# Performance work log

Hardware: AMD Instinct MI355X
Metric: run time of the kernel (lower is better)

## Reference

```python
import jax, jax.numpy as jnp
import numpy as np

N, F_IN, H = 8192, 128, 256
AVG_DEG_P = 16.0 / N  # ~16 neighbors per node, BA-graph-like sparsity


def setup_inputs() -> dict:
    key = jax.random.key(0)
    ks = jax.random.split(key, 16)
    # symmetric 0/1 adjacency, no self-loops
    B = jax.random.bernoulli(ks[0], AVG_DEG_P, (N, N)).astype(jnp.float32)
    A = jnp.maximum(B, B.T)
    A = A * (1.0 - jnp.eye(N, dtype=jnp.float32))
    features = jax.random.normal(ks[1], (N, F_IN), dtype=jnp.float32)
    treatments = jax.random.bernoulli(ks[2], 0.1, (N, 1)).astype(jnp.float32)
    def glorot(k, shape):
        lim = float(np.sqrt(6.0 / (shape[0] + shape[1])))
        return jax.random.uniform(k, shape, jnp.float32, -lim, lim)
    return {
        "A": A,
        "features": features,
        "treatments": treatments,
        "W1": glorot(ks[3], (F_IN, H)),   # GCNConv layer 1 weight
        "b1": jnp.zeros((H,), jnp.float32),
        "W2": glorot(ks[4], (H, H)),      # GCNConv layer 2 weight
        "b2": jnp.zeros((H,), jnp.float32),
        "W_emb": glorot(ks[5], (H + 1, H)),
        "b_emb": jnp.zeros((H,), jnp.float32),
        "W_t0": glorot(ks[6], (H, 1)),
        "b_t0": jnp.zeros((1,), jnp.float32),
        "W_t1": glorot(ks[7], (H, 1)),
        "b_t1": jnp.zeros((1,), jnp.float32),
    }


def _gcn_norm(A):
    # PyG GCNConv default: D^-1/2 (A + I) D^-1/2
    A_hat = A + jnp.eye(A.shape[0], dtype=A.dtype)
    d = jnp.sum(A_hat, axis=1)
    dinv = jnp.where(d > 0, 1.0 / jnp.sqrt(d), 0.0)
    return A_hat * dinv[:, None] * dinv[None, :]


def reference(A, features, treatments, W1, b1, W2, b2, W_emb, b_emb, W_t0, b_t0, W_t1, b_t1):
    nA = _gcn_norm(A)                                  # [N, N]
    h = jax.nn.relu(nA @ (features @ W1) + b1)         # GCNConv 1, [N, H]
    h = jax.nn.relu(nA @ (h @ W2) + b2)                # GCNConv 2, [N, H]
    deg = jnp.sum(A, axis=1) + 1e-8                    # [N]
    # faithful to torch: (A * treatments).sum(dim=1) broadcasts treatments[N,1] over columns
    exposure = (jnp.sum(A * treatments, axis=1) / deg)[:, None]  # [N, 1]
    rep = jnp.concatenate([h, exposure], axis=1)       # [N, H+1]
    emb = jax.nn.relu(rep @ W_emb + b_emb)             # [N, H]
    y0_pred = (emb @ W_t0 + b_t0).reshape(-1)          # [N]
    y1_pred = (emb @ W_t1 + b_t1).reshape(-1)          # [N]
    return (y0_pred, y1_pred, emb)
```

## Files before the change

### kernel.cpp

```cpp
#include <hip/hip_runtime.h>

#define NN   8192
#define FIN  128
#define HH   256
#define CAP  128

__global__ __launch_bounds__(256) void k_build(
    const float* __restrict__ A, const float* __restrict__ treat,
    int* __restrict__ cols, int* __restrict__ cnt,
    float* __restrict__ dinv, float* __restrict__ expo)
{
  const int row = blockIdx.x;
  const float4* Ar = reinterpret_cast<const float4*>(A + (size_t)row * NN);
  __shared__ int s_cnt;
  __shared__ float s_rs[4];
  if (threadIdx.x == 0) s_cnt = 0;
  __syncthreads();

  float rs = 0.f;
  int* myCols = cols + (size_t)row * CAP;
  #pragma unroll
  for (int it = 0; it < NN / 4 / 256; ++it) {
    const int idx = it * 256 + threadIdx.x;
    const float4 a = Ar[idx];
    const int base = idx * 4;
    const float av[4] = {a.x, a.y, a.z, a.w};
    #pragma unroll
    for (int u = 0; u < 4; ++u) {
      if (av[u] != 0.0f) {
        rs += av[u];
        int p = atomicAdd(&s_cnt, 1);
        if (p < CAP) myCols[p] = base + u;
      }
    }
  }
  #pragma unroll
  for (int off = 32; off > 0; off >>= 1) rs += __shfl_down(rs, off);
  const int wid = threadIdx.x >> 6;
  if ((threadIdx.x & 63) == 0) s_rs[wid] = rs;
  __syncthreads();
  if (threadIdx.x == 0) {
    const float R = s_rs[0] + s_rs[1] + s_rs[2] + s_rs[3];
    int n = s_cnt; if (n > CAP) n = CAP;
    cnt[row]  = n;
    dinv[row] = rsqrtf(R + 1.0f);
    expo[row] = treat[row] * R / (R + 1e-8f);
  }
}

template<int K, bool EXPO>
__global__ __launch_bounds__(256) void k_gemm(
    const float* __restrict__ M, const float* __restrict__ W,
    const float* __restrict__ bias, const float* __restrict__ expo,
    float* __restrict__ out)
{
  constexpr int BM = 128, BN = 64, KT = 16;
  __shared__ float As[KT][BM];
  __shared__ float Bs[KT][BN];
  const int tid = threadIdx.x;
  const int tx = tid & 15;
  const int ty = tid >> 4;
  const int r0 = blockIdx.x * BM;
  const int c0 = blockIdx.y * BN;

  float acc[8][4];
  #pragma unroll
  for (int i = 0; i < 8; ++i)
    #pragma unroll
    for (int j = 0; j < 4; ++j) acc[i][j] = 0.f;

  const int lr = tid >> 1;
  const int lk = (tid & 1) * 8;
  const int bk = tid >> 4;
  const int bc = (tid & 15) * 4;

  for (int k0 = 0; k0 < K; k0 += KT) {
    const float4 a0 = *reinterpret_cast<const float4*>(&M[(size_t)(r0 + lr) * K + k0 + lk]);
    const float4 a1 = *reinterpret_cast<const float4*>(&M[(size_t)(r0 + lr) * K + k0 + lk + 4]);
    const float4 b0 = *reinterpret_cast<const float4*>(&W[(size_t)(k0 + bk) * HH + c0 + bc]);
    __syncthreads();
    As[lk + 0][lr] = a0.x; As[lk + 1][lr] = a0.y; As[lk + 2][lr] = a0.z; As[lk + 3][lr] = a0.w;
    As[lk + 4][lr] = a1.x; As[lk + 5][lr] = a1.y; As[lk + 6][lr] = a1.z; As[lk + 7][lr] = a1.w;
    *reinterpret_cast<float4*>(&Bs[bk][bc]) = b0;
    __syncthreads();
    #pragma unroll
    for (int kk = 0; kk < KT; ++kk) {
      const float4 av0 = *reinterpret_cast<const float4*>(&As[kk][ty * 8]);
      const float4 av1 = *reinterpret_cast<const float4*>(&As[kk][ty * 8 + 4]);
      const float4 bv  = *reinterpret_cast<const float4*>(&Bs[kk][tx * 4]);
      const float ar[8] = {av0.x, av0.y, av0.z, av0.w, av1.x, av1.y, av1.z, av1.w};
      const float br[4] = {bv.x, bv.y, bv.z, bv.w};
      #pragma unroll
      for (int i = 0; i < 8; ++i)
        #pragma unroll
        for (int j = 0; j < 4; ++j)
          acc[i][j] += ar[i] * br[j];
    }
  }

  float eb[4] = {0, 0, 0, 0}, bs[4] = {0, 0, 0, 0};
  if constexpr (EXPO) {
    const float4 we = *reinterpret_cast<const float4*>(&W[(size_t)K * HH + c0 + tx * 4]);
    eb[0] = we.x; eb[1] = we.y; eb[2] = we.z; eb[3] = we.w;
    const float4 bv = *reinterpret_cast<const float4*>(&bias[c0 + tx * 4]);
    bs[0] = bv.x; bs[1] = bv.y; bs[2] = bv.z; bs[3] = bv.w;
  }
  #pragma unroll
  for (int i = 0; i < 8; ++i) {
    const int r = r0 + ty * 8 + i;
    float4 o;
    float ov[4];
    if constexpr (EXPO) {
      const float e = expo[r];
      #pragma unroll
      for (int j = 0; j < 4; ++j) ov[j] = fmaxf(acc[i][j] + e * eb[j] + bs[j], 0.f);
    } else {
      #pragma unroll
      for (int j = 0; j < 4; ++j) ov[j] = acc[i][j];
    }
    o.x = ov[0]; o.y = ov[1]; o.z = ov[2]; o.w = ov[3];
    *reinterpret_cast<float4*>(&out[(size_t)r * HH + c0 + tx * 4]) = o;
  }
}

__global__ __launch_bounds__(256) void k_agg(
    const float* __restrict__ M,
    const int* __restrict__ cols, const int* __restrict__ cnt,
    const float* __restrict__ dinv, const float* __restrict__ bias,
    float* __restrict__ out)
{
  const int i = blockIdx.x;
  const int c = threadIdx.x;
  __shared__ int   s_cols[CAP];
  __shared__ float s_w[CAP];
  const int n = cnt[i];
  for (int t = threadIdx.x; t < n; t += 256) {
    const int j = cols[(size_t)i * CAP + t];
    s_cols[t] = j;
    s_w[t] = dinv[j];
  }
  __syncthreads();
  const float di = dinv[i];
  float acc = di * M[(size_t)i * HH + c];
  #pragma unroll 4
  for (int t = 0; t < n; ++t)
    acc += s_w[t] * M[(size_t)s_cols[t] * HH + c];
  const float v = di * acc + bias[c];
  out[(size_t)i * HH + c] = fmaxf(v, 0.f);
}

__global__ __launch_bounds__(64) void k_heads(
    const float* __restrict__ emb,
    const float* __restrict__ Wt0, const float* __restrict__ bt0,
    const float* __restrict__ Wt1, const float* __restrict__ bt1,
    float* __restrict__ y0, float* __restrict__ y1)
{
  const int i = blockIdx.x;
  const int l = threadIdx.x;
  float s0 = 0.f, s1 = 0.f;
  #pragma unroll
  for (int c = l; c < HH; c += 64) {
    const float e = emb[(size_t)i * HH + c];
    s0 += e * Wt0[c];
    s1 += e * Wt1[c];
  }
  #pragma unroll
  for (int off = 32; off > 0; off >>= 1) {
    s0 += __shfl_down(s0, off);
    s1 += __shfl_down(s1, off);
  }
  if (l == 0) {
    y0[i] = s0 + bt0[0];
    y1[i] = s1 + bt1[0];
  }
}

extern "C" void kernel_launch(void* const* d_in, const int* in_sizes, int n_in,
                              void* d_out, int out_size, void* d_ws, size_t ws_size,
                              hipStream_t stream)
{
  const float* A      = (const float*)d_in[0];
  const float* feats  = (const float*)d_in[1];
  const float* treat  = (const float*)d_in[2];
  const float* W1     = (const float*)d_in[3];
  const float* b1     = (const float*)d_in[4];
  const float* W2     = (const float*)d_in[5];
  const float* b2     = (const float*)d_in[6];
  const float* W_emb  = (const float*)d_in[7];
  const float* b_emb  = (const float*)d_in[8];
  const float* W_t0   = (const float*)d_in[9];
  const float* b_t0   = (const float*)d_in[10];
  const float* W_t1   = (const float*)d_in[11];
  const float* b_t1   = (const float*)d_in[12];
  float* dout = (float*)d_out;

  int*   cols = (int*)d_ws;
  int*   cnt  = cols + (size_t)NN * CAP;
  float* dinv = (float*)(cnt + NN);
  float* expo = dinv + NN;
  float* bufA = expo + NN;
  float* bufB = bufA + (size_t)NN * HH;

  float* y0  = dout;
  float* y1  = dout + NN;
  float* emb = dout + 2 * NN;

  const dim3 gemmGrid(NN / 128, HH / 64);

  k_build<<<NN, 256, 0, stream>>>(A, treat, cols, cnt, dinv, expo);
  k_gemm<FIN, false><<<gemmGrid, 256, 0, stream>>>(feats, W1, nullptr, nullptr, bufA);
  k_agg<<<NN, 256, 0, stream>>>(bufA, cols, cnt, dinv, b1, bufB);
  k_gemm<HH, false><<<gemmGrid, 256, 0, stream>>>(bufB, W2, nullptr, nullptr, bufA);
  k_agg<<<NN, 256, 0, stream>>>(bufA, cols, cnt, dinv, b2, bufB);
  k_gemm<HH, true><<<gemmGrid, 256, 0, stream>>>(bufB, W_emb, b_emb, expo, emb);
  k_heads<<<NN, 64, 0, stream>>>(emb, W_t0, b_t0, W_t1, b_t1, y0, y1);
}
```

Before: 519.0 us.

## Fuse aggregation with GEMMs per 16-row block and reorder layer-1 as aggregate-then-transform

Replaces the six-kernel GEMM/aggregate/heads pipeline with two fused kernels. Each block handles 16 nodes, gathers neighbor rows into LDS, and multiplies by the weight tile. Layer 1 now aggregates the 128-wide features before multiplying by W1, which reduces gather width. Layer 2, the embedding GEMM and both heads run in one kernel, removing intermediate global round-trips and launches. The adjacency scan also uses nontemporal loads. In exchange, the small 16-row tiles reuse the weights less, reload W from global for every block, and may limit occupancy because of the large LDS footprint.

```diff
diff --git a/kernel.cpp b/kernel.cpp
--- a/kernel.cpp
+++ b/kernel.cpp
@@ -4,6 +4,16 @@
 #define FIN  128
 #define HH   256
 #define CAP  128
+#define BND  16
+#define NBLK (NN / BND)
+
+typedef float f32x4 __attribute__((ext_vector_type(4)));
+typedef float f32x2 __attribute__((ext_vector_type(2)));
+
+__device__ __forceinline__ const f32x4* c4(const float* p) { return (const f32x4*)p; }
+__device__ __forceinline__       f32x4* p4(float* p)       { return (f32x4*)p; }
+__device__ __forceinline__ const f32x2* c2(const float* p) { return (const f32x2*)p; }
+__device__ __forceinline__       f32x2* p2(float* p)       { return (f32x2*)p; }
 
 __global__ __launch_bounds__(256) void k_build(
     const float* __restrict__ A, const float* __restrict__ treat,
@@ -11,8 +21,8 @@
     float* __restrict__ dinv, float* __restrict__ expo)
 {
   const int row = blockIdx.x;
-  const float4* Ar = reinterpret_cast<const float4*>(A + (size_t)row * NN);
-  __shared__ int s_cnt;
+  const f32x4* Ar = c4(A + (size_t)row * NN);
+  __shared__ int   s_cnt;
   __shared__ float s_rs[4];
   if (threadIdx.x == 0) s_cnt = 0;
   __syncthreads();
@@ -22,13 +32,12 @@
   #pragma unroll
   for (int it = 0; it < NN / 4 / 256; ++it) {
     const int idx = it * 256 + threadIdx.x;
-    const float4 a = Ar[idx];
+    const f32x4 a = __builtin_nontemporal_load(Ar + idx);
     const int base = idx * 4;
-    const float av[4] = {a.x, a.y, a.z, a.w};
     #pragma unroll
     for (int u = 0; u < 4; ++u) {
-      if (av[u] != 0.0f) {
-        rs += av[u];
+      if (a[u] != 0.0f) {
+        rs += a[u];
         int p = atomicAdd(&s_cnt, 1);
         if (p < CAP) myCols[p] = base + u;
       }
@@ -48,130 +57,189 @@
   }
 }
 
-template<int K, bool EXPO>
-__global__ __launch_bounds__(256) void k_gemm(
-    const float* __restrict__ M, const float* __restrict__ W,
-    const float* __restrict__ bias, const float* __restrict__ expo,
-    float* __restrict__ out)
-{
-  constexpr int BM = 128, BN = 64, KT = 16;
-  __shared__ float As[KT][BM];
-  __shared__ float Bs[KT][BN];
+template<int K>
+__device__ __forceinline__ void gemm_tile(
+    const float* __restrict__ hbase, int hstride,
+    const float* __restrict__ W, float (*w_lds)[HH + 4],
+    int ty, int tx, int tid, float acc[4][4])
+{
+  #pragma unroll 1
+  for (int k0 = 0; k0 < K; k0 += 16) {
+    __syncthreads();
+    #pragma unroll
+    for (int rr = 0; rr < 4; ++rr) {
+      const int flat = rr * 1024 + tid * 4;
+      const int row = flat >> 8, col = flat & 255;
+      *p4(&w_lds[row][col]) = *c4(&W[(size_t)(k0 + row) * HH + col]);
+    }
+    __syncthreads();
+    #pragma unroll
+    for (int kk4 = 0; kk4 < 4; ++kk4) {
+      f32x4 a4[4];
+      #pragma unroll
+      for (int i = 0; i < 4; ++i)
+        a4[i] = *c4(&hbase[(size_t)(4 * ty + i) * hstride + k0 + 4 * kk4]);
+      #pragma unroll
+      for (int q = 0; q < 4; ++q) {
+        const f32x4 b4 = *c4(&w_lds[4 * kk4 + q][4 * tx]);
+        #pragma unroll
+        for (int i = 0; i < 4; ++i)
+          #pragma unroll
+          for (int j = 0; j < 4; ++j)
+            acc[i][j] += a4[i][q] * b4[j];
+      }
+    }
+  }
+}
+
+__global__ __launch_bounds__(256) void k_fused1(
+    const float* __restrict__ X, const int* __restrict__ cols,
+    const int* __restrict__ cnt, const float* __restrict__ dinv,
+    const float* __restrict__ W1, const float* __restrict__ b1,
+    float* __restrict__ h1)
+{
+  __shared__ float h_lds[BND][FIN + 4];
+  __shared__ float w_lds[16][HH + 4];
+  __shared__ int   s_cnt[BND];
+  __shared__ int   s_colsG[BND][CAP];
+  __shared__ float s_wG[BND][CAP];
+
   const int tid = threadIdx.x;
-  const int tx = tid & 15;
-  const int ty = tid >> 4;
-  const int r0 = blockIdx.x * BM;
-  const int c0 = blockIdx.y * BN;
-
-  float acc[8][4];
-  #pragma unroll
-  for (int i = 0; i < 8; ++i)
-    #pragma unroll
-    for (int j = 0; j < 4; ++j) acc[i][j] = 0.f;
-
-  const int lr = tid >> 1;
-  const int lk = (tid & 1) * 8;
-  const int bk = tid >> 4;
-  const int bc = (tid & 15) * 4;
-
-  for (int k0 = 0; k0 < K; k0 += KT) {
-    const float4 a0 = *reinterpret_cast<const float4*>(&M[(size_t)(r0 + lr) * K + k0 + lk]);
-    const float4 a1 = *reinterpret_cast<const float4*>(&M[(size_t)(r0 + lr) * K + k0 + lk + 4]);
-    const float4 b0 = *reinterpret_cast<const float4*>(&W[(size_t)(k0 + bk) * HH + c0 + bc]);
-    __syncthreads();
-    As[lk + 0][lr] = a0.x; As[lk + 1][lr] = a0.y; As[lk + 2][lr] = a0.z; As[lk + 3][lr] = a0.w;
-    As[lk + 4][lr] = a1.x; As[lk + 5][lr] = a1.y; As[lk + 6][lr] = a1.z; As[lk + 7][lr] = a1.w;
-    *reinterpret_cast<float4*>(&Bs[bk][bc]) = b0;
-    __syncthreads();
-    #pragma unroll
-    for (int kk = 0; kk < KT; ++kk) {
-      const float4 av0 = *reinterpret_cast<const float4*>(&As[kk][ty * 8]);
-      const float4 av1 = *reinterpret_cast<const float4*>(&As[kk][ty * 8 + 4]);
-      const float4 bv  = *reinterpret_cast<const float4*>(&Bs[kk][tx * 4]);
-      const float ar[8] = {av0.x, av0.y, av0.z, av0.w, av1.x, av1.y, av1.z, av1.w};
-      const float br[4] = {bv.x, bv.y, bv.z, bv.w};
-      #pragma unroll
-      for (int i = 0; i < 8; ++i)
-        #pragma unroll
-        for (int j = 0; j < 4; ++j)
-          acc[i][j] += ar[i] * br[j];
-    }
-  }
-
-  float eb[4] = {0, 0, 0, 0}, bs[4] = {0, 0, 0, 0};
-  if constexpr (EXPO) {
-    const float4 we = *reinterpret_cast<const float4*>(&W[(size_t)K * HH + c0 + tx * 4]);
-    eb[0] = we.x; eb[1] = we.y; eb[2] = we.z; eb[3] = we.w;
-    const float4 bv = *reinterpret_cast<const float4*>(&bias[c0 + tx * 4]);
-    bs[0] = bv.x; bs[1] = bv.y; bs[2] = bv.z; bs[3] = bv.w;
-  }
-  #pragma unroll
-  for (int i = 0; i < 8; ++i) {
-    const int r = r0 + ty * 8 + i;
-    float4 o;
-    float ov[4];
-    if constexpr (EXPO) {
-      const float e = expo[r];
-      #pragma unroll
-      for (int j = 0; j < 4; ++j) ov[j] = fmaxf(acc[i][j] + e * eb[j] + bs[j], 0.f);
-    } else {
-      #pragma unroll
-      for (int j = 0; j < 4; ++j) ov[j] = acc[i][j];
-    }
-    o.x = ov[0]; o.y = ov[1]; o.z = ov[2]; o.w = ov[3];
-    *reinterpret_cast<float4*>(&out[(size_t)r * HH + c0 + tx * 4]) = o;
-  }
-}
-
-__global__ __launch_bounds__(256) void k_agg(
-    const float* __restrict__ M,
-    const int* __restrict__ cols, const int* __restrict__ cnt,
-    const float* __restrict__ dinv, const float* __restrict__ bias,
-    float* __restrict__ out)
-{
-  const int i = blockIdx.x;
-  const int c = threadIdx.x;
-  __shared__ int   s_cols[CAP];
-  __shared__ float s_w[CAP];
-  const int n = cnt[i];
-  for (int t = threadIdx.x; t < n; t += 256) {
-    const int j = cols[(size_t)i * CAP + t];
-    s_cols[t] = j;
-    s_w[t] = dinv[j];
-  }
-  __syncthreads();
-  const float di = dinv[i];
-  float acc = di * M[(size_t)i * HH + c];
-  #pragma unroll 4
-  for (int t = 0; t < n; ++t)
-    acc += s_w[t] * M[(size_t)s_cols[t] * HH + c];
-  const float v = di * acc + bias[c];
-  out[(size_t)i * HH + c] = fmaxf(v, 0.f);
-}
-
-__global__ __launch_bounds__(64) void k_heads(
-    const float* __restrict__ emb,
-    const float* __restrict__ Wt0, const float* __restrict__ bt0,
-    const float* __restrict__ Wt1, const float* __restrict__ bt1,
-    float* __restrict__ y0, float* __restrict__ y1)
-{
-  const int i = blockIdx.x;
-  const int l = threadIdx.x;
-  float s0 = 0.f, s1 = 0.f;
-  #pragma unroll
-  for (int c = l; c < HH; c += 64) {
-    const float e = emb[(size_t)i * HH + c];
-    s0 += e * Wt0[c];
-    s1 += e * Wt1[c];
-  }
-  #pragma unroll
-  for (int off = 32; off > 0; off >>= 1) {
-    s0 += __shfl_down(s0, off);
-    s1 += __shfl_down(s1, off);
-  }
-  if (l == 0) {
-    y0[i] = s0 + bt0[0];
-    y1[i] = s1 + bt1[0];
+  const int ty = tid >> 6, tx = tid & 63;
+  const int r0 = blockIdx.x * BND;
+
+  if (tid < BND) s_cnt[tid] = cnt[r0 + tid];
+  __syncthreads();
+  for (int e = tid; e < BND * CAP; e += 256) {
+    const int node = e >> 7, t = e & (CAP - 1);
+    if (t < s_cnt[node]) {
+      const int j = cols[(size_t)(r0 + node) * CAP + t];
+      s_colsG[node][t] = j;
+      s_wG[node][t]    = dinv[j];
+    }
+  }
+  __syncthreads();
+
+  #pragma unroll 1
+  for (int s = 0; s < 4; ++s) {
+    const int lr = ty * 4 + s;
+    const int i  = r0 + lr;
+    const float di = dinv[i];
+    const int n = s_cnt[lr];
+    f32x2 acc = *c2(&X[(size_t)i * FIN + 2 * tx]);
+    acc *= di;
+    #pragma unroll 4
+    for (int t = 0; t < n; ++t) {
+      const int   j = s_colsG[lr][t];
+      const float w = s_wG[lr][t];
+      acc += w * (*c2(&X[(size_t)j * FIN + 2 * tx]));
+    }
+    *p2(&h_lds[lr][2 * tx]) = di * acc;
+  }
+
+  float acc[4][4] = {};
+  gemm_tile<FIN>(&h_lds[0][0], FIN + 4, W1, w_lds, ty, tx, tid, acc);
+
+  const f32x4 bs = *c4(&b1[4 * tx]);
+  #pragma unroll
+  for (int i = 0; i < 4; ++i) {
+    const int r = r0 + 4 * ty + i;
+    f32x4 o;
+    #pragma unroll
+    for (int j = 0; j < 4; ++j) o[j] = fmaxf(acc[i][j] + bs[j], 0.f);
+    *p4(&h1[(size_t)r * HH + 4 * tx]) = o;
+  }
+}
+
+__global__ __launch_bounds__(256) void k_mega(
+    const float* __restrict__ H1, const int* __restrict__ cols,
+    const int* __restrict__ cnt, const float* __restrict__ dinv,
+    const float* __restrict__ expo,
+    const float* __restrict__ W2, const float* __restrict__ b2,
+    const float* __restrict__ W_emb, const float* __restrict__ b_emb,
+    const float* __restrict__ W_t0, const float* __restrict__ b_t0,
+    const float* __restrict__ W_t1, const float* __restrict__ b_t1,
+    float* __restrict__ emb, float* __restrict__ y0, float* __restrict__ y1)
+{
+  __shared__ float h_lds[BND][HH + 4];
+  __shared__ float g_lds[BND][HH + 4];
+  __shared__ float w_lds[16][HH + 4];
+  __shared__ int   s_cnt[BND];
+  __shared__ int   s_colsG[BND][CAP];
+  __shared__ float s_wG[BND][CAP];
+
+  const int tid = threadIdx.x;
+  const int ty = tid >> 6, tx = tid & 63;
+  const int r0 = blockIdx.x * BND;
+
+  if (tid < BND) s_cnt[tid] = cnt[r0 + tid];
+  __syncthreads();
+  for (int e = tid; e < BND * CAP; e += 256) {
+    const int node = e >> 7, t = e & (CAP - 1);
+    if (t < s_cnt[node]) {
+      const int j = cols[(size_t)(r0 + node) * CAP + t];
+      s_colsG[node][t] = j;
+      s_wG[node][t]    = dinv[j];
+    }
+  }
+  __syncthreads();
+
+  #pragma unroll 1
+  for (int s = 0; s < 4; ++s) {
+    const int lr = ty * 4 + s;
+    const int i  = r0 + lr;
+    const float di = dinv[i];
+    const int n = s_cnt[lr];
+    f32x4 acc = *c4(&H1[(size_t)i * HH + 4 * tx]);
+    acc *= di;
+    #pragma unroll 4
+    for (int t = 0; t < n; ++t) {
+      const int   j = s_colsG[lr][t];
+      const float w = s_wG[lr][t];
+      acc += w * (*c4(&H1[(size_t)j * HH + 4 * tx]));
+    }
+    *p4(&h_lds[lr][4 * tx]) = di * acc;
+  }
+
+  float acc[4][4] = {};
+  gemm_tile<HH>(&h_lds[0][0], HH + 4, W2, w_lds, ty, tx, tid, acc);
+  {
+    const f32x4 bs = *c4(&b2[4 * tx]);
+    #pragma unroll
+    for (int i = 0; i < 4; ++i) {
+      f32x4 o;
+      #pragma unroll
+      for (int j = 0; j < 4; ++j) o[j] = fmaxf(acc[i][j] + bs[j], 0.f);
+      *p4(&g_lds[4 * ty + i][4 * tx]) = o;
+      #pragma unroll
+      for (int j = 0; j < 4; ++j) acc[i][j] = 0.f;
+    }
+  }
+
+  gemm_tile<HH>(&g_lds[0][0], HH + 4, W_emb, w_lds, ty, tx, tid, acc);
+
+  const f32x4 eb  = *c4(&W_emb[(size_t)HH * HH + 4 * tx]);
+  const f32x4 bse = *c4(&b_emb[4 * tx]);
+  const f32x4 wt0 = *c4(&W_t0[4 * tx]);
+  const f32x4 wt1 = *c4(&W_t1[4 * tx]);
+  const float bt0 = b_t0[0], bt1 = b_t1[0];
+  #pragma unroll
+  for (int i = 0; i < 4; ++i) {
+    const int r = r0 + 4 * ty + i;
+    const float e = expo[r];
+    f32x4 o;
+    #pragma unroll
+    for (int j = 0; j < 4; ++j)
+      o[j] = fmaxf(acc[i][j] + e * eb[j] + bse[j], 0.f);
+    *p4(&emb[(size_t)r * HH + 4 * tx]) = o;
+    float s0 = o[0]*wt0[0] + o[1]*wt0[1] + o[2]*wt0[2] + o[3]*wt0[3];
+    float s1 = o[0]*wt1[0] + o[1]*wt1[1] + o[2]*wt1[2] + o[3]*wt1[3];
+    #pragma unroll
+    for (int off = 32; off > 0; off >>= 1) {
+      s0 += __shfl_down(s0, off);
+      s1 += __shfl_down(s1, off);
+    }
+    if (tx == 0) { y0[r] = s0 + bt0; y1[r] = s1 + bt1; }
   }
 }
 
@@ -198,20 +266,15 @@
   int*   cnt  = cols + (size_t)NN * CAP;
   float* dinv = (float*)(cnt + NN);
   float* expo = dinv + NN;
-  float* bufA = expo + NN;
-  float* bufB = bufA + (size_t)NN * HH;
+  float* bufH = expo + NN;
 
   float* y0  = dout;
   float* y1  = dout + NN;
   float* emb = dout + 2 * NN;
 
-  const dim3 gemmGrid(NN / 128, HH / 64);
-
   k_build<<<NN, 256, 0, stream>>>(A, treat, cols, cnt, dinv, expo);
-  k_gemm<FIN, false><<<gemmGrid, 256, 0, stream>>>(feats, W1, nullptr, nullptr, bufA);
-  k_agg<<<NN, 256, 0, stream>>>(bufA, cols, cnt, dinv, b1, bufB);
-  k_gemm<HH, false><<<gemmGrid, 256, 0, stream>>>(bufB, W2, nullptr, nullptr, bufA);
-  k_agg<<<NN, 256, 0, stream>>>(bufA, cols, cnt, dinv, b2, bufB);
-  k_gemm<HH, true><<<gemmGrid, 256, 0, stream>>>(bufB, W_emb, b_emb, expo, emb);
-  k_heads<<<NN, 64, 0, stream>>>(emb, W_t0, b_t0, W_t1, b_t1, y0, y1);
-}
+  k_fused1<<<NBLK, 256, 0, stream>>>(feats, cols, cnt, dinv, W1, b1, bufH);
+  k_mega<<<NBLK, 256, 0, stream>>>(bufH, cols, cnt, dinv, expo,
+                                   W2, b2, W_emb, b_emb, W_t0, b_t0, W_t1, b_t1,
+                                   emb, y0, y1);
+}
```

Measured after the change: 459.0 us. 1.13x faster.
